# Kernel tuning notes

Measured on AMD Instinct MI355X. Metric: run time of the kernel, lower is better.

Reference implementation:

```python
import jax, jax.numpy as jnp
import numpy as np

B, T, D, R, C = 8, 4096, 128, 8, 128
LN_EPS = 1e-5


def _mlp(x, A1, c1, A2, c2):
    # Linear -> GELU(exact, erf-based like torch nn.GELU default) -> Linear
    return jax.nn.gelu(x @ A1 + c1, approximate=False) @ A2 + c2


def setup_inputs() -> dict:
    key = jax.random.key(0)
    ks = jax.random.split(key, 12)
    s = 0.02
    f32 = jnp.float32
    return {
        "cells_state": jax.random.normal(ks[0], (B, T, D), f32),
        "c_state": jax.random.normal(ks[1], (C,), f32),
        # 8 rule MLPs stacked: Linear(3D->2D), GELU, Linear(2D->D), Tanh
        "W1": (jax.random.normal(ks[2], (R, 3 * D, 2 * D), f32) * s),
        "b1": jnp.zeros((R, 2 * D), f32),
        "W2": (jax.random.normal(ks[3], (R, 2 * D, D), f32) * s),
        "b2": jnp.zeros((R, D), f32),
        # rule selector: c_dim -> 64 -> n_rules
        "rsel_W1": jax.random.normal(ks[4], (C, 64), f32) * s,
        "rsel_b1": jnp.zeros((64,), f32),
        "rsel_W2": jax.random.normal(ks[5], (64, R), f32) * s,
        "rsel_b2": jnp.zeros((R,), f32),
        # steps selector: c_dim -> 32 -> 7
        "ssel_W1": jax.random.normal(ks[6], (C, 32), f32) * s,
        "ssel_b1": jnp.zeros((32,), f32),
        "ssel_W2": jax.random.normal(ks[7], (32, 7), f32) * s,
        "ssel_b2": jnp.zeros((7,), f32),
        # residual selector: c_dim -> 32 -> 1 -> sigmoid
        "asel_W1": jax.random.normal(ks[8], (C, 32), f32) * s,
        "asel_b1": jnp.zeros((32,), f32),
        "asel_W2": jax.random.normal(ks[9], (32, 1), f32) * s,
        "asel_b2": jnp.zeros((1,), f32),
        # LayerNorm(d_model)
        "ln_g": jnp.ones((D,), f32),
        "ln_b": jnp.zeros((D,), f32),
    }


def reference(cells_state, c_state, W1, b1, W2, b2,
              rsel_W1, rsel_b1, rsel_W2, rsel_b2,
              ssel_W1, ssel_b1, ssel_W2, ssel_b2,
              asel_W1, asel_b1, asel_W2, asel_b2,
              ln_g, ln_b):
    rule_weights = jax.nn.softmax(_mlp(c_state, rsel_W1, rsel_b1, rsel_W2, rsel_b2))
    steps_w = jax.nn.softmax(_mlp(c_state, ssel_W1, ssel_b1, ssel_W2, ssel_b2))
    possible_steps = jnp.arange(2.0, 9.0, dtype=jnp.float32)  # [2..8]
    n_soft = jnp.sum(steps_w * possible_steps)
    # torch does int(n_soft.item() + 0.5) on the host -> fixed Python loop count
    n_evolve = max(2, min(8, int(float(n_soft) + 0.5)))
    alpha = 0.1 + 0.8 * jax.nn.sigmoid(
        _mlp(c_state, asel_W1, asel_b1, asel_W2, asel_b2))[0]

    for _ in range(n_evolve):
        left = jnp.roll(cells_state, 1, axis=1)
        right = jnp.roll(cells_state, -1, axis=1)
        rule_input = jnp.concatenate([cells_state, left, right], axis=-1)  # [B,T,3D]
        # all 8 rule MLPs as one grouped GEMM pair
        h = jax.nn.gelu(
            jnp.einsum('btk,rkh->rbth', rule_input, W1) + b1[:, None, None, :],
            approximate=False)                                             # [R,B,T,2D]
        rules_out = jnp.tanh(
            jnp.einsum('rbth,rhd->rbtd', h, W2) + b2[:, None, None, :])    # [R,B,T,D]
        new_cells = jnp.einsum('r,rbtd->btd', rule_weights, rules_out)
        cells_state = alpha * cells_state + (1.0 - alpha) * new_cells

    mu = jnp.mean(cells_state, axis=-1, keepdims=True)
    var = jnp.var(cells_state, axis=-1, keepdims=True)
    out = (cells_state - mu) / jnp.sqrt(var + LN_EPS) * ln_g + ln_b
    return out
```

## Files before the change

kernel.cpp:

```cpp
#include <hip/hip_runtime.h>
#include <math.h>

#define T_ 4096
#define D_ 128
#define R_ 8

#define LDS_BARRIER() asm volatile("s_waitcnt lgkmcnt(0)\n\ts_barrier" ::: "memory")

typedef float f32x4 __attribute__((ext_vector_type(4)));
typedef _Float16 f16x8 __attribute__((ext_vector_type(8)));
typedef unsigned short u16x8 __attribute__((ext_vector_type(8)));

__device__ __forceinline__ unsigned short f2h_bits(float f) {
    _Float16 h = (_Float16)f;
    return __builtin_bit_cast(unsigned short, h);
}

__device__ __forceinline__ unsigned long long pack4h(float a, float b, float c, float d) {
    unsigned int lo = __builtin_bit_cast(unsigned int, __builtin_amdgcn_cvt_pkrtz(a, b));
    unsigned int hi = __builtin_bit_cast(unsigned int, __builtin_amdgcn_cvt_pkrtz(c, d));
    return ((unsigned long long)hi << 32) | (unsigned long long)lo;
}

__device__ __forceinline__ float tanh_fast(float x) {
    float e = __builtin_amdgcn_exp2f(x * 2.885390082f);
    float r = __builtin_amdgcn_rcpf(e + 1.0f);
    return fmaf(-2.0f, r, 1.0f);
}

__device__ __forceinline__ float gelu_fast(float x) {
    float x2 = x * x;
    float u = x * fmaf(x2, 0.044715f, 1.0f);
    float e = __builtin_amdgcn_exp2f(u * -2.3022082f);
    return x * __builtin_amdgcn_rcpf(1.0f + e);
}

__device__ __forceinline__ float gelu_exact(float x) {
    return 0.5f * x * (1.0f + erff(x * 0.7071067811865475f));
}

__global__ void selectors_kernel(
    const float* __restrict__ c,
    const float* __restrict__ rW1, const float* __restrict__ rb1,
    const float* __restrict__ rW2, const float* __restrict__ rb2,
    const float* __restrict__ sW1, const float* __restrict__ sb1,
    const float* __restrict__ sW2, const float* __restrict__ sb2,
    const float* __restrict__ aW1, const float* __restrict__ ab1,
    const float* __restrict__ aW2, const float* __restrict__ ab2,
    float* __restrict__ hdr)
{
    __shared__ float cs[128];
    __shared__ float hb[64];
    __shared__ float lg[8];
    const int l = threadIdx.x;
    cs[l] = c[l];
    cs[l + 64] = c[l + 64];
    __syncthreads();

    {
        float acc = rb1[l];
        for (int k = 0; k < 128; ++k) acc += cs[k] * rW1[k * 64 + l];
        hb[l] = gelu_exact(acc);
    }
    __syncthreads();
    if (l < 8) {
        float acc = rb2[l];
        for (int j = 0; j < 64; ++j) acc += hb[j] * rW2[j * 8 + l];
        lg[l] = acc;
    }
    __syncthreads();
    if (l == 0) {
        float mx = lg[0];
        for (int o = 1; o < 8; ++o) mx = fmaxf(mx, lg[o]);
        float e[8], se = 0.0f;
        for (int o = 0; o < 8; ++o) { e[o] = expf(lg[o] - mx); se += e[o]; }
        for (int o = 0; o < 8; ++o) hdr[2 + o] = e[o] / se;
    }
    __syncthreads();

    if (l < 32) {
        float acc = sb1[l];
        for (int k = 0; k < 128; ++k) acc += cs[k] * sW1[k * 32 + l];
        hb[l] = gelu_exact(acc);
    }
    __syncthreads();
    if (l < 7) {
        float acc = sb2[l];
        for (int j = 0; j < 32; ++j) acc += hb[j] * sW2[j * 7 + l];
        lg[l] = acc;
    }
    __syncthreads();
    if (l == 0) {
        float mx = lg[0];
        for (int o = 1; o < 7; ++o) mx = fmaxf(mx, lg[o]);
        float e[7], se = 0.0f;
        for (int o = 0; o < 7; ++o) { e[o] = expf(lg[o] - mx); se += e[o]; }
        float n_soft = 0.0f;
        for (int o = 0; o < 7; ++o) n_soft += (e[o] / se) * (float)(2 + o);
        int ne = (int)floorf(n_soft + 0.5f);
        ne = ne < 2 ? 2 : (ne > 8 ? 8 : ne);
        hdr[0] = (float)ne;
    }
    __syncthreads();

    if (l < 32) {
        float acc = ab1[l];
        for (int k = 0; k < 128; ++k) acc += cs[k] * aW1[k * 32 + l];
        hb[l] = gelu_exact(acc);
    }
    __syncthreads();
    if (l == 0) {
        float acc = ab2[0];
        for (int j = 0; j < 32; ++j) acc += hb[j] * aW2[j];
        hdr[1] = 0.1f + 0.8f / (1.0f + expf(-acc));
    }
}

__global__ __launch_bounds__(256) void prep_weights(
    const float* __restrict__ W1, const float* __restrict__ W2,
    unsigned short* __restrict__ W1F, unsigned short* __restrict__ W2F)
{
    const int bx = blockIdx.x;
    const int t = threadIdx.x;
    if (bx < 96) {
        const int r = bx / 12;
        const int kk = bx % 12;
        unsigned short* dst = W1F + (size_t)bx * 8192;
#pragma unroll
        for (int i = 0; i < 4; ++i) {
            const int idx = i * 256 + t;
            const int nb = idx >> 6;
            const int lane = idx & 63;
            const int n = nb * 16 + (lane & 15);
            const int k0 = kk * 32 + (lane >> 4) * 8;
            u16x8 v;
#pragma unroll
            for (int j = 0; j < 8; ++j)
                v[j] = f2h_bits(W1[((size_t)r * 384 + k0 + j) * 256 + n]);
            *reinterpret_cast<u16x8*>(dst + idx * 8) = v;
        }
    } else {
        const int b2 = bx - 96;
        const int r = b2 >> 3;
        const int k2 = b2 & 7;
        unsigned short* dst = W2F + (size_t)b2 * 4096;
#pragma unroll
        for (int i = 0; i < 2; ++i) {
            const int idx = i * 256 + t;
            const int nb = idx >> 6;
            const int lane = idx & 63;
            const int n = nb * 16 + (lane & 15);
            const int k0 = k2 * 32 + (lane >> 4) * 8;
            u16x8 v;
#pragma unroll
            for (int j = 0; j < 8; ++j)
                v[j] = f2h_bits(W2[((size_t)r * 256 + k0 + j) * 128 + n]);
            *reinterpret_cast<u16x8*>(dst + idx * 8) = v;
        }
    }
}

__global__ __launch_bounds__(512, 2) void evolve_step(
    int step,
    const float* __restrict__ cells_in,
    float* __restrict__ buf0,
    float* __restrict__ buf1,
    const unsigned short* __restrict__ W1F,
    const unsigned short* __restrict__ W2F,
    const float* __restrict__ b1,
    const float* __restrict__ b2,
    const float* __restrict__ hdr)
{
    if (step >= (int)hdr[0]) return;
    const float* src = (step == 0) ? cells_in : ((step & 1) ? buf0 : buf1);
    float* dst = (step & 1) ? buf1 : buf0;
    const float alpha = hdr[1];

    __shared__ __align__(16) unsigned short Xs[66 * 128];
    __shared__ __align__(16) unsigned short Hs[64 * 256];

    const int tid = threadIdx.x;
    const int blk = blockIdx.x;
    const int b = blk >> 6;
    const int t0 = (blk & 63) << 6;
    const float* srcb = src + (size_t)b * (T_ * D_);

    {
        const int cr = (tid & 31) << 2;
        for (int j = (tid >> 5); j < 66; j += 16) {
            const int tg = (t0 + j - 1) & (T_ - 1);
            const f32x4 v = *reinterpret_cast<const f32x4*>(srcb + tg * D_ + cr);
            int byte = (j * 128 + cr) * 2;
            byte ^= (j & 7) << 4;
            *reinterpret_cast<unsigned long long*>(reinterpret_cast<char*>(Xs) + byte) =
                pack4h(v[0], v[1], v[2], v[3]);
        }
    }
    __syncthreads();

    const int wave = tid >> 6;
    const int lane = tid & 63;
    const int l16 = lane & 15;
    const int lhi = lane >> 4;
    const int kbase = lhi * 8;
    const char* Xsb = reinterpret_cast<const char*>(Xs);
    char* Hsb = reinterpret_cast<char*>(Hs);

    const f32x4 z4 = {0.0f, 0.0f, 0.0f, 0.0f};
    f32x4 facc[4];
#pragma unroll
    for (int bq = 0; bq < 4; ++bq) facc[bq] = z4;

    const int lane8 = lane * 8;

#pragma unroll 1
    for (int r = 0; r < R_; ++r) {
        const unsigned short* w1r = W1F + (size_t)r * (12 * 8192) + (size_t)(wave * 2) * 512 + lane8;
        const unsigned short* w2r = W2F + (size_t)r * (8 * 4096) + (size_t)wave * 512 + lane8;

        f16x8 w1f[12][2];
#pragma unroll
        for (int kk = 0; kk < 12; ++kk) {
            const size_t off = (size_t)kk * 8192;
            w1f[kk][0] = __builtin_bit_cast(f16x8, *reinterpret_cast<const u16x8*>(w1r + off));
            w1f[kk][1] = __builtin_bit_cast(f16x8, *reinterpret_cast<const u16x8*>(w1r + off + 512));
        }
        f16x8 wfr2[3];
        wfr2[0] = __builtin_bit_cast(f16x8, *reinterpret_cast<const u16x8*>(w2r));
        wfr2[1] = __builtin_bit_cast(f16x8, *reinterpret_cast<const u16x8*>(w2r + 4096));
        f32x4 bv1[2], bv2;
        bv1[0] = *reinterpret_cast<const f32x4*>(b1 + r * 256 + wave * 32 + lhi * 4);
        bv1[1] = *reinterpret_cast<const f32x4*>(b1 + r * 256 + wave * 32 + 16 + lhi * 4);
        bv2    = *reinterpret_cast<const f32x4*>(b2 + r * 128 + wave * 16 + lhi * 4);

        f16x8 xfr[2][4], hfr[2][4];
#pragma unroll
        for (int tf = 0; tf < 4; ++tf) {
            const int row = tf * 16 + l16 + 1;
            int byte = row * 256 + kbase * 2;
            byte ^= (row & 7) << 4;
            xfr[0][tf] = __builtin_bit_cast(f16x8,
                *reinterpret_cast<const u16x8*>(Xsb + byte));
        }

        f32x4 acc1[2][4];
#pragma unroll
        for (int a = 0; a < 2; ++a)
#pragma unroll
            for (int bq = 0; bq < 4; ++bq) acc1[a][bq] = z4;

#pragma unroll
        for (int kk = 0; kk < 12; ++kk) {
            if (kk < 11) {
                const int kn = kk + 1;
                const int segn = kn >> 2;
                const int rowaddn = (segn == 0) ? 1 : ((segn == 1) ? 0 : 2);
                const int klocn = ((kn & 3) * 32 + kbase) * 2;
#pragma unroll
                for (int tf = 0; tf < 4; ++tf) {
                    const int row = tf * 16 + l16 + rowaddn;
                    int byte = row * 256 + klocn;
                    byte ^= (row & 7) << 4;
                    xfr[(kk + 1) & 1][tf] = __builtin_bit_cast(f16x8,
                        *reinterpret_cast<const u16x8*>(Xsb + byte));
                }
            }
#pragma unroll
            for (int nf = 0; nf < 2; ++nf)
#pragma unroll
                for (int tf = 0; tf < 4; ++tf)
                    acc1[nf][tf] = __builtin_amdgcn_mfma_f32_16x16x32_f16(
                        w1f[kk][nf], xfr[kk & 1][tf], acc1[nf][tf], 0, 0, 0);
        }

        LDS_BARRIER();

#pragma unroll
        for (int tf = 0; tf < 4; ++tf) {
            const int t = tf * 16 + l16;
            const int rowbyte = t * 512;
            const int swz = (t & 7) << 4;
#pragma unroll
            for (int nf = 0; nf < 2; ++nf) {
                const f32x4 a = acc1[nf][tf];
                const float g0 = gelu_fast(a[0] + bv1[nf][0]);
                const float g1 = gelu_fast(a[1] + bv1[nf][1]);
                const float g2 = gelu_fast(a[2] + bv1[nf][2]);
                const float g3 = gelu_fast(a[3] + bv1[nf][3]);
                int byte = rowbyte + wave * 64 + nf * 32 + lhi * 8;
                byte ^= swz;
                *reinterpret_cast<unsigned long long*>(Hsb + byte) =
                    pack4h(g0, g1, g2, g3);
            }
        }
        LDS_BARRIER();

        f32x4 acc2[4];
#pragma unroll
        for (int bq = 0; bq < 4; ++bq) acc2[bq] = z4;

#pragma unroll
        for (int tf = 0; tf < 4; ++tf) {
            const int t = tf * 16 + l16;
            int byte = t * 512 + kbase * 2;
            byte ^= (t & 7) << 4;
            hfr[0][tf] = __builtin_bit_cast(f16x8,
                *reinterpret_cast<const u16x8*>(Hsb + byte));
        }

#pragma unroll
        for (int k2 = 0; k2 < 8; ++k2) {
            if (k2 < 6) {
                wfr2[(k2 + 2) % 3] = __builtin_bit_cast(f16x8,
                    *reinterpret_cast<const u16x8*>(w2r + (size_t)(k2 + 2) * 4096));
            }
            if (k2 < 7) {
                const int kgn = ((k2 + 1) * 32 + kbase) * 2;
#pragma unroll
                for (int tf = 0; tf < 4; ++tf) {
                    const int t = tf * 16 + l16;
                    int byte = t * 512 + kgn;
                    byte ^= (t & 7) << 4;
                    hfr[(k2 + 1) & 1][tf] = __builtin_bit_cast(f16x8,
                        *reinterpret_cast<const u16x8*>(Hsb + byte));
                }
            }
#pragma unroll
            for (int tf = 0; tf < 4; ++tf)
                acc2[tf] = __builtin_amdgcn_mfma_f32_16x16x32_f16(
                    wfr2[k2 % 3], hfr[k2 & 1][tf], acc2[tf], 0, 0, 0);
        }

        const float rw = hdr[2 + r];
#pragma unroll
        for (int tf = 0; tf < 4; ++tf)
#pragma unroll
            for (int i = 0; i < 4; ++i)
                facc[tf][i] += rw * tanh_fast(acc2[tf][i] + bv2[i]);
    }

    float* dstb = dst + (size_t)b * (T_ * D_);
    const float om = 1.0f - alpha;
    const int c0 = wave * 16 + lhi * 4;
#pragma unroll
    for (int tf = 0; tf < 4; ++tf) {
        const int t = t0 + tf * 16 + l16;
        const size_t idx = (size_t)t * D_ + c0;
        const f32x4 x = *reinterpret_cast<const f32x4*>(srcb + idx);
        f32x4 o;
#pragma unroll
        for (int i = 0; i < 4; ++i) o[i] = alpha * x[i] + om * facc[tf][i];
        *reinterpret_cast<f32x4*>(dstb + idx) = o;
    }
}

__global__ __launch_bounds__(256) void ln_kernel(
    const float* __restrict__ buf0, const float* __restrict__ buf1,
    const float* __restrict__ hdr,
    const float* __restrict__ g, const float* __restrict__ bb,
    float* __restrict__ out)
{
    const int ne = (int)hdr[0];
    const float* src = ((ne - 1) & 1) ? buf1 : buf0;
    const int row = blockIdx.x * 4 + (threadIdx.x >> 6);
    const int lane = threadIdx.x & 63;
    const size_t base = (size_t)row * D_;
    const int d = lane * 2;
    const float a = src[base + d];
    const float c = src[base + d + 1];
    float s = a + c;
    float q = a * a + c * c;
#pragma unroll
    for (int off = 32; off >= 1; off >>= 1) {
        s += __shfl_xor(s, off);
        q += __shfl_xor(q, off);
    }
    const float mean = s * (1.0f / 128.0f);
    float var = q * (1.0f / 128.0f) - mean * mean;
    var = fmaxf(var, 0.0f);
    const float rstd = rsqrtf(var + 1e-5f);
    out[base + d]     = (a - mean) * rstd * g[d] + bb[d];
    out[base + d + 1] = (c - mean) * rstd * g[d + 1] + bb[d + 1];
}

extern "C" void kernel_launch(void* const* d_in, const int* in_sizes, int n_in,
                              void* d_out, int out_size, void* d_ws, size_t ws_size,
                              hipStream_t stream)
{
    (void)in_sizes; (void)n_in; (void)out_size; (void)ws_size;
    const float* cells  = (const float*)d_in[0];
    const float* cst    = (const float*)d_in[1];
    const float* W1     = (const float*)d_in[2];
    const float* b1     = (const float*)d_in[3];
    const float* W2     = (const float*)d_in[4];
    const float* b2     = (const float*)d_in[5];
    const float* rW1    = (const float*)d_in[6];
    const float* rb1    = (const float*)d_in[7];
    const float* rW2    = (const float*)d_in[8];
    const float* rb2    = (const float*)d_in[9];
    const float* sW1    = (const float*)d_in[10];
    const float* sb1    = (const float*)d_in[11];
    const float* sW2    = (const float*)d_in[12];
    const float* sb2    = (const float*)d_in[13];
    const float* aW1    = (const float*)d_in[14];
    const float* ab1    = (const float*)d_in[15];
    const float* aW2    = (const float*)d_in[16];
    const float* ab2    = (const float*)d_in[17];
    const float* ln_g   = (const float*)d_in[18];
    const float* ln_b   = (const float*)d_in[19];
    float* out = (float*)d_out;

    char* ws = (char*)d_ws;
    float* hdr  = (float*)ws;
    float* buf0 = (float*)(ws + 256);
    unsigned short* W1F = (unsigned short*)(ws + 256 + 16777216);
    unsigned short* W2F = W1F + (size_t)96 * 8192;
    float* buf1 = out;

    hipLaunchKernelGGL(prep_weights, dim3(160), dim3(256), 0, stream, W1, W2, W1F, W2F);
    hipLaunchKernelGGL(selectors_kernel, dim3(1), dim3(64), 0, stream,
                       cst, rW1, rb1, rW2, rb2, sW1, sb1, sW2, sb2,
                       aW1, ab1, aW2, ab2, hdr);
    for (int s = 0; s < 8; ++s) {
        hipLaunchKernelGGL(evolve_step, dim3(512), dim3(512), 0, stream,
                           s, cells, buf0, buf1, W1F, W2F, b1, b2, hdr);
    }
    hipLaunchKernelGGL(ln_kernel, dim3(8192), dim3(256), 0, stream,
                       buf0, buf1, hdr, ln_g, ln_b, out);
}
```

Baseline: 618.4 us.

## Switch evolve GEMMs to 32x32x16 MFMA with 4-wave blocks and streamed weights

Replaces the 16x16x32 MFMA tiling with 32x32x16 MFMA, halving the block to 4 waves that each own 64 hidden / 32 output columns. W1 fragments are now streamed from global memory with a 3-deep rotating prefetch instead of all 24 being preloaded into registers. The prep kernel is relaid out to match the new fragment format. MFMA sections are wrapped in s_setprio to favour matrix issue. Larger MFMA tiles reduce LDS fragment reads per flop, but fewer waves per block and in-loop global weight loads may expose latency.

```diff
diff --git a/kernel.cpp b/kernel.cpp
--- a/kernel.cpp
+++ b/kernel.cpp
@@ -8,6 +8,7 @@
 #define LDS_BARRIER() asm volatile("s_waitcnt lgkmcnt(0)\n\ts_barrier" ::: "memory")
 
 typedef float f32x4 __attribute__((ext_vector_type(4)));
+typedef float f32x16 __attribute__((ext_vector_type(16)));
 typedef _Float16 f16x8 __attribute__((ext_vector_type(8)));
 typedef unsigned short u16x8 __attribute__((ext_vector_type(8)));
 
@@ -122,45 +123,39 @@
 {
     const int bx = blockIdx.x;
     const int t = threadIdx.x;
-    if (bx < 96) {
-        const int r = bx / 12;
-        const int kk = bx % 12;
-        unsigned short* dst = W1F + (size_t)bx * 8192;
-#pragma unroll
-        for (int i = 0; i < 4; ++i) {
-            const int idx = i * 256 + t;
-            const int nb = idx >> 6;
-            const int lane = idx & 63;
-            const int n = nb * 16 + (lane & 15);
-            const int k0 = kk * 32 + (lane >> 4) * 8;
-            u16x8 v;
-#pragma unroll
-            for (int j = 0; j < 8; ++j)
-                v[j] = f2h_bits(W1[((size_t)r * 384 + k0 + j) * 256 + n]);
-            *reinterpret_cast<u16x8*>(dst + idx * 8) = v;
-        }
-    } else {
-        const int b2 = bx - 96;
-        const int r = b2 >> 3;
-        const int k2 = b2 & 7;
-        unsigned short* dst = W2F + (size_t)b2 * 4096;
+    if (bx < 192) {
+        const int r = bx / 24;
+        const int ks = bx % 24;
 #pragma unroll
         for (int i = 0; i < 2; ++i) {
             const int idx = i * 256 + t;
             const int nb = idx >> 6;
             const int lane = idx & 63;
-            const int n = nb * 16 + (lane & 15);
-            const int k0 = k2 * 32 + (lane >> 4) * 8;
+            const int n = nb * 32 + (lane & 31);
+            const int k0 = ks * 16 + (lane >> 5) * 8;
             u16x8 v;
 #pragma unroll
             for (int j = 0; j < 8; ++j)
-                v[j] = f2h_bits(W2[((size_t)r * 256 + k0 + j) * 128 + n]);
-            *reinterpret_cast<u16x8*>(dst + idx * 8) = v;
-        }
-    }
-}
-
-__global__ __launch_bounds__(512, 2) void evolve_step(
+                v[j] = f2h_bits(W1[((size_t)r * 384 + k0 + j) * 256 + n]);
+            *reinterpret_cast<u16x8*>(W1F + ((size_t)bx * 8 + nb) * 512 + lane * 8) = v;
+        }
+    } else {
+        const int b2 = bx - 192;
+        const int r = b2 / 16;
+        const int ks = b2 % 16;
+        const int nb = t >> 6;
+        const int lane = t & 63;
+        const int n = nb * 32 + (lane & 31);
+        const int k0 = ks * 16 + (lane >> 5) * 8;
+        u16x8 v;
+#pragma unroll
+        for (int j = 0; j < 8; ++j)
+            v[j] = f2h_bits(W2[((size_t)r * 256 + k0 + j) * 128 + n]);
+        *reinterpret_cast<u16x8*>(W2F + ((size_t)b2 * 4 + nb) * 512 + lane * 8) = v;
+    }
+}
+
+__global__ __launch_bounds__(256, 2) void evolve_step(
     int step,
     const float* __restrict__ cells_in,
     float* __restrict__ buf0,
@@ -187,7 +182,7 @@
 
     {
         const int cr = (tid & 31) << 2;
-        for (int j = (tid >> 5); j < 66; j += 16) {
+        for (int j = (tid >> 5); j < 66; j += 8) {
             const int tg = (t0 + j - 1) & (T_ - 1);
             const f32x4 v = *reinterpret_cast<const f32x4*>(srcb + tg * D_ + cr);
             int byte = (j * 128 + cr) * 2;
@@ -200,157 +195,186 @@
 
     const int wave = tid >> 6;
     const int lane = tid & 63;
-    const int l16 = lane & 15;
-    const int lhi = lane >> 4;
-    const int kbase = lhi * 8;
+    const int l32 = lane & 31;
+    const int lk = lane >> 5;
     const char* Xsb = reinterpret_cast<const char*>(Xs);
     char* Hsb = reinterpret_cast<char*>(Hs);
 
-    const f32x4 z4 = {0.0f, 0.0f, 0.0f, 0.0f};
-    f32x4 facc[4];
-#pragma unroll
-    for (int bq = 0; bq < 4; ++bq) facc[bq] = z4;
+    f32x16 facc[2];
+#pragma unroll
+    for (int tb = 0; tb < 2; ++tb)
+#pragma unroll
+        for (int i = 0; i < 16; ++i) facc[tb][i] = 0.0f;
 
     const int lane8 = lane * 8;
 
 #pragma unroll 1
     for (int r = 0; r < R_; ++r) {
-        const unsigned short* w1r = W1F + (size_t)r * (12 * 8192) + (size_t)(wave * 2) * 512 + lane8;
-        const unsigned short* w2r = W2F + (size_t)r * (8 * 4096) + (size_t)wave * 512 + lane8;
-
-        f16x8 w1f[12][2];
-#pragma unroll
-        for (int kk = 0; kk < 12; ++kk) {
-            const size_t off = (size_t)kk * 8192;
-            w1f[kk][0] = __builtin_bit_cast(f16x8, *reinterpret_cast<const u16x8*>(w1r + off));
-            w1f[kk][1] = __builtin_bit_cast(f16x8, *reinterpret_cast<const u16x8*>(w1r + off + 512));
-        }
+        const unsigned short* w1r = W1F + ((size_t)r * 24 * 8 + wave * 2) * 512 + lane8;
+        const unsigned short* w2r = W2F + ((size_t)r * 16 * 4 + wave) * 512 + lane8;
+
+        f16x8 w1f[3][2];
         f16x8 wfr2[3];
-        wfr2[0] = __builtin_bit_cast(f16x8, *reinterpret_cast<const u16x8*>(w2r));
-        wfr2[1] = __builtin_bit_cast(f16x8, *reinterpret_cast<const u16x8*>(w2r + 4096));
-        f32x4 bv1[2], bv2;
-        bv1[0] = *reinterpret_cast<const f32x4*>(b1 + r * 256 + wave * 32 + lhi * 4);
-        bv1[1] = *reinterpret_cast<const f32x4*>(b1 + r * 256 + wave * 32 + 16 + lhi * 4);
-        bv2    = *reinterpret_cast<const f32x4*>(b2 + r * 128 + wave * 16 + lhi * 4);
-
-        f16x8 xfr[2][4], hfr[2][4];
-#pragma unroll
-        for (int tf = 0; tf < 4; ++tf) {
-            const int row = tf * 16 + l16 + 1;
-            int byte = row * 256 + kbase * 2;
+        f16x8 xfr[2][2];
+        f16x8 hfr[2][2];
+        f32x4 bv1[2][4], bv2[4];
+
+        w1f[0][0] = __builtin_bit_cast(f16x8, *reinterpret_cast<const u16x8*>(w1r));
+        w1f[0][1] = __builtin_bit_cast(f16x8, *reinterpret_cast<const u16x8*>(w1r + 512));
+        w1f[1][0] = __builtin_bit_cast(f16x8, *reinterpret_cast<const u16x8*>(w1r + 4096));
+        w1f[1][1] = __builtin_bit_cast(f16x8, *reinterpret_cast<const u16x8*>(w1r + 4096 + 512));
+        wfr2[0]   = __builtin_bit_cast(f16x8, *reinterpret_cast<const u16x8*>(w2r));
+        wfr2[1]   = __builtin_bit_cast(f16x8, *reinterpret_cast<const u16x8*>(w2r + 2048));
+#pragma unroll
+        for (int nb = 0; nb < 2; ++nb)
+#pragma unroll
+            for (int q = 0; q < 4; ++q)
+                bv1[nb][q] = *reinterpret_cast<const f32x4*>(
+                    b1 + r * 256 + wave * 64 + nb * 32 + q * 8 + lk * 4);
+#pragma unroll
+        for (int q = 0; q < 4; ++q)
+            bv2[q] = *reinterpret_cast<const f32x4*>(
+                b2 + r * 128 + wave * 32 + q * 8 + lk * 4);
+#pragma unroll
+        for (int tb = 0; tb < 2; ++tb) {
+            const int row = tb * 32 + l32 + 1;
+            int byte = row * 256 + lk * 16;
             byte ^= (row & 7) << 4;
-            xfr[0][tf] = __builtin_bit_cast(f16x8,
+            xfr[0][tb] = __builtin_bit_cast(f16x8,
                 *reinterpret_cast<const u16x8*>(Xsb + byte));
         }
 
-        f32x4 acc1[2][4];
-#pragma unroll
-        for (int a = 0; a < 2; ++a)
-#pragma unroll
-            for (int bq = 0; bq < 4; ++bq) acc1[a][bq] = z4;
-
-#pragma unroll
-        for (int kk = 0; kk < 12; ++kk) {
-            if (kk < 11) {
-                const int kn = kk + 1;
-                const int segn = kn >> 2;
-                const int rowaddn = (segn == 0) ? 1 : ((segn == 1) ? 0 : 2);
-                const int klocn = ((kn & 3) * 32 + kbase) * 2;
-#pragma unroll
-                for (int tf = 0; tf < 4; ++tf) {
-                    const int row = tf * 16 + l16 + rowaddn;
-                    int byte = row * 256 + klocn;
+        f32x16 acc1[2][2];
+#pragma unroll
+        for (int nb = 0; nb < 2; ++nb)
+#pragma unroll
+            for (int tb = 0; tb < 2; ++tb)
+#pragma unroll
+                for (int i = 0; i < 16; ++i) acc1[nb][tb][i] = 0.0f;
+
+#pragma unroll
+        for (int ks = 0; ks < 24; ++ks) {
+            if (ks < 22) {
+                const size_t off = (size_t)(ks + 2) * 4096;
+                w1f[(ks + 2) % 3][0] = __builtin_bit_cast(f16x8,
+                    *reinterpret_cast<const u16x8*>(w1r + off));
+                w1f[(ks + 2) % 3][1] = __builtin_bit_cast(f16x8,
+                    *reinterpret_cast<const u16x8*>(w1r + off + 512));
+            }
+            if (ks < 23) {
+                const int kn = ks + 1;
+                const int seg = kn >> 3;
+                const int rowadd = (seg == 0) ? 1 : ((seg == 1) ? 0 : 2);
+                const int kloc = (kn & 7) * 32 + lk * 16;
+#pragma unroll
+                for (int tb = 0; tb < 2; ++tb) {
+                    const int row = tb * 32 + l32 + rowadd;
+                    int byte = row * 256 + kloc;
                     byte ^= (row & 7) << 4;
-                    xfr[(kk + 1) & 1][tf] = __builtin_bit_cast(f16x8,
+                    xfr[(ks + 1) & 1][tb] = __builtin_bit_cast(f16x8,
                         *reinterpret_cast<const u16x8*>(Xsb + byte));
                 }
             }
-#pragma unroll
-            for (int nf = 0; nf < 2; ++nf)
-#pragma unroll
-                for (int tf = 0; tf < 4; ++tf)
-                    acc1[nf][tf] = __builtin_amdgcn_mfma_f32_16x16x32_f16(
-                        w1f[kk][nf], xfr[kk & 1][tf], acc1[nf][tf], 0, 0, 0);
+            __builtin_amdgcn_s_setprio(1);
+#pragma unroll
+            for (int nb = 0; nb < 2; ++nb)
+#pragma unroll
+                for (int tb = 0; tb < 2; ++tb)
+                    acc1[nb][tb] = __builtin_amdgcn_mfma_f32_32x32x16_f16(
+                        w1f[ks % 3][nb], xfr[ks & 1][tb], acc1[nb][tb], 0, 0, 0);
+            __builtin_amdgcn_s_setprio(0);
         }
 
         LDS_BARRIER();
 
 #pragma unroll
-        for (int tf = 0; tf < 4; ++tf) {
-            const int t = tf * 16 + l16;
+        for (int tb = 0; tb < 2; ++tb) {
+            const int t = tb * 32 + l32;
             const int rowbyte = t * 512;
             const int swz = (t & 7) << 4;
 #pragma unroll
-            for (int nf = 0; nf < 2; ++nf) {
-                const f32x4 a = acc1[nf][tf];
-                const float g0 = gelu_fast(a[0] + bv1[nf][0]);
-                const float g1 = gelu_fast(a[1] + bv1[nf][1]);
-                const float g2 = gelu_fast(a[2] + bv1[nf][2]);
-                const float g3 = gelu_fast(a[3] + bv1[nf][3]);
-                int byte = rowbyte + wave * 64 + nf * 32 + lhi * 8;
-                byte ^= swz;
-                *reinterpret_cast<unsigned long long*>(Hsb + byte) =
-                    pack4h(g0, g1, g2, g3);
+            for (int nb = 0; nb < 2; ++nb) {
+#pragma unroll
+                for (int q = 0; q < 4; ++q) {
+                    const float g0 = gelu_fast(acc1[nb][tb][q * 4 + 0] + bv1[nb][q][0]);
+                    const float g1 = gelu_fast(acc1[nb][tb][q * 4 + 1] + bv1[nb][q][1]);
+                    const float g2 = gelu_fast(acc1[nb][tb][q * 4 + 2] + bv1[nb][q][2]);
+                    const float g3 = gelu_fast(acc1[nb][tb][q * 4 + 3] + bv1[nb][q][3]);
+                    int byte = rowbyte + (wave * 64 + nb * 32 + q * 8 + lk * 4) * 2;
+                    byte ^= swz;
+                    *reinterpret_cast<unsigned long long*>(Hsb + byte) =
+                        pack4h(g0, g1, g2, g3);
+                }
             }
         }
         LDS_BARRIER();
 
-        f32x4 acc2[4];
-#pragma unroll
-        for (int bq = 0; bq < 4; ++bq) acc2[bq] = z4;
-
-#pragma unroll
-        for (int tf = 0; tf < 4; ++tf) {
-            const int t = tf * 16 + l16;
-            int byte = t * 512 + kbase * 2;
+        f32x16 acc2[2];
+#pragma unroll
+        for (int tb = 0; tb < 2; ++tb)
+#pragma unroll
+            for (int i = 0; i < 16; ++i) acc2[tb][i] = 0.0f;
+
+#pragma unroll
+        for (int tb = 0; tb < 2; ++tb) {
+            const int t = tb * 32 + l32;
+            int byte = t * 512 + lk * 16;
             byte ^= (t & 7) << 4;
-            hfr[0][tf] = __builtin_bit_cast(f16x8,
+            hfr[0][tb] = __builtin_bit_cast(f16x8,
                 *reinterpret_cast<const u16x8*>(Hsb + byte));
         }
 
 #pragma unroll
-        for (int k2 = 0; k2 < 8; ++k2) {
-            if (k2 < 6) {
-                wfr2[(k2 + 2) % 3] = __builtin_bit_cast(f16x8,
-                    *reinterpret_cast<const u16x8*>(w2r + (size_t)(k2 + 2) * 4096));
+        for (int ks = 0; ks < 16; ++ks) {
+            if (ks < 14) {
+                wfr2[(ks + 2) % 3] = __builtin_bit_cast(f16x8,
+                    *reinterpret_cast<const u16x8*>(w2r + (size_t)(ks + 2) * 2048));
             }
-            if (k2 < 7) {
-                const int kgn = ((k2 + 1) * 32 + kbase) * 2;
-#pragma unroll
-                for (int tf = 0; tf < 4; ++tf) {
-                    const int t = tf * 16 + l16;
-                    int byte = t * 512 + kgn;
+            if (ks < 15) {
+                const int kloc = (ks + 1) * 32 + lk * 16;
+#pragma unroll
+                for (int tb = 0; tb < 2; ++tb) {
+                    const int t = tb * 32 + l32;
+                    int byte = t * 512 + kloc;
                     byte ^= (t & 7) << 4;
-                    hfr[(k2 + 1) & 1][tf] = __builtin_bit_cast(f16x8,
+                    hfr[(ks + 1) & 1][tb] = __builtin_bit_cast(f16x8,
                         *reinterpret_cast<const u16x8*>(Hsb + byte));
                 }
             }
-#pragma unroll
-            for (int tf = 0; tf < 4; ++tf)
-                acc2[tf] = __builtin_amdgcn_mfma_f32_16x16x32_f16(
-                    wfr2[k2 % 3], hfr[k2 & 1][tf], acc2[tf], 0, 0, 0);
+            __builtin_amdgcn_s_setprio(1);
+#pragma unroll
+            for (int tb = 0; tb < 2; ++tb)
+                acc2[tb] = __builtin_amdgcn_mfma_f32_32x32x16_f16(
+                    wfr2[ks % 3], hfr[ks & 1][tb], acc2[tb], 0, 0, 0);
+            __builtin_amdgcn_s_setprio(0);
         }
 
         const float rw = hdr[2 + r];
 #pragma unroll
-        for (int tf = 0; tf < 4; ++tf)
-#pragma unroll
-            for (int i = 0; i < 4; ++i)
-                facc[tf][i] += rw * tanh_fast(acc2[tf][i] + bv2[i]);
+        for (int tb = 0; tb < 2; ++tb)
+#pragma unroll
+            for (int q = 0; q < 4; ++q)
+#pragma unroll
+                for (int i = 0; i < 4; ++i)
+                    facc[tb][q * 4 + i] += rw * tanh_fast(acc2[tb][q * 4 + i] + bv2[q][i]);
     }
 
     float* dstb = dst + (size_t)b * (T_ * D_);
     const float om = 1.0f - alpha;
-    const int c0 = wave * 16 + lhi * 4;
-#pragma unroll
-    for (int tf = 0; tf < 4; ++tf) {
-        const int t = t0 + tf * 16 + l16;
-        const size_t idx = (size_t)t * D_ + c0;
-        const f32x4 x = *reinterpret_cast<const f32x4*>(srcb + idx);
-        f32x4 o;
-#pragma unroll
-        for (int i = 0; i < 4; ++i) o[i] = alpha * x[i] + om * facc[tf][i];
-        *reinterpret_cast<f32x4*>(dstb + idx) = o;
+#pragma unroll
+    for (int tb = 0; tb < 2; ++tb) {
+        const int t = t0 + tb * 32 + l32;
+#pragma unroll
+        for (int q = 0; q < 4; ++q) {
+            const int n0 = wave * 32 + q * 8 + lk * 4;
+            const size_t idx = (size_t)t * D_ + n0;
+            const f32x4 x = *reinterpret_cast<const f32x4*>(srcb + idx);
+            f32x4 o;
+#pragma unroll
+            for (int i = 0; i < 4; ++i)
+                o[i] = alpha * x[i] + om * facc[tb][q * 4 + i];
+            *reinterpret_cast<f32x4*>(dstb + idx) = o;
+        }
     }
 }
 
@@ -414,15 +438,15 @@
     float* hdr  = (float*)ws;
     float* buf0 = (float*)(ws + 256);
     unsigned short* W1F = (unsigned short*)(ws + 256 + 16777216);
-    unsigned short* W2F = W1F + (size_t)96 * 8192;
+    unsigned short* W2F = W1F + (size_t)192 * 4096;
     float* buf1 = out;
 
-    hipLaunchKernelGGL(prep_weights, dim3(160), dim3(256), 0, stream, W1, W2, W1F, W2F);
+    hipLaunchKernelGGL(prep_weights, dim3(320), dim3(256), 0, stream, W1, W2, W1F, W2F);
     hipLaunchKernelGGL(selectors_kernel, dim3(1), dim3(64), 0, stream,
                        cst, rW1, rb1, rW2, rb2, sW1, sb1, sW2, sb2,
                        aW1, ab1, aW2, ab2, hdr);
     for (int s = 0; s < 8; ++s) {
-        hipLaunchKernelGGL(evolve_step, dim3(512), dim3(512), 0, stream,
+        hipLaunchKernelGGL(evolve_step, dim3(512), dim3(256), 0, stream,
                            s, cells, buf0, buf1, W1F, W2F, b1, b2, hdr);
     }
     hipLaunchKernelGGL(ln_kernel, dim3(8192), dim3(256), 0, stream,
```

New measurement: 654.3 us. +5.8%, slower.
